# Performance work log

Hardware: AMD Instinct MI355X
Metric: run time of the kernel (lower is better)

## Reference

```python
import jax, jax.numpy as jnp
import numpy as np

N = 50000      # nodes
E = 800000     # edges (before self-loops)
F_IN = 128     # num_node_features
G = 128        # number of graphs in batch
NEG_SLOPE = 0.2  # PyG GATConv leaky_relu slope


def _add_self_loops(src, dst, n):
    loop = jnp.arange(n, dtype=src.dtype)
    return jnp.concatenate([src, loop]), jnp.concatenate([dst, loop])


def gcn_conv(x, W, b, src, dst, n):
    h = x @ W
    deg = jax.ops.segment_sum(jnp.ones_like(dst, dtype=h.dtype), dst, num_segments=n)
    dinv = jnp.where(deg > 0, jax.lax.rsqrt(deg), 0.0)
    norm = dinv[src] * dinv[dst]                      # [E+N]
    msg = h[src] * norm[:, None]                      # gather + scale
    return jax.ops.segment_sum(msg, dst, num_segments=n) + b


def gat_conv(x, W, att_src, att_dst, b, src, dst, n, heads, ch):
    # PyG GATConv (concat=True, self-loops added by caller)
    h = (x @ W).reshape(n, heads, ch)                 # [N,H,C]
    a_src = (h * att_src).sum(-1)                     # [N,H]
    a_dst = (h * att_dst).sum(-1)                     # [N,H]
    e = jax.nn.leaky_relu(a_src[src] + a_dst[dst], NEG_SLOPE)  # [E+N,H]
    # segment softmax over edges grouped by destination
    m = jax.ops.segment_max(e, dst, num_segments=n)   # [N,H]
    ex = jnp.exp(e - m[dst])
    s = jax.ops.segment_sum(ex, dst, num_segments=n)  # [N,H]
    alpha = ex / s[dst]                               # [E+N,H]
    msg = h[src] * alpha[:, :, None]                  # [E+N,H,C]
    out = jax.ops.segment_sum(msg, dst, num_segments=n)
    return out.reshape(n, heads * ch) + b


def setup_inputs() -> dict:
    key = jax.random.key(0)
    ks = jax.random.split(key, 16)
    p = lambda k, shape: jax.random.normal(k, shape, jnp.float32) * 0.05
    return {
        "x": jax.random.normal(ks[0], (N, F_IN), jnp.float32),
        "edge_index": jax.random.randint(ks[1], (2, E), 0, N, dtype=jnp.int32),
        "batch": jnp.sort(jax.random.randint(ks[2], (N,), 0, G, dtype=jnp.int32)),
        "W1": p(ks[3], (F_IN, 16)), "b1": jnp.zeros((16,), jnp.float32),
        "W2": p(ks[4], (16, 32)), "b2": jnp.zeros((32,), jnp.float32),
        "W3": p(ks[5], (32, 4 * 32)), "att_src3": p(ks[6], (4, 32)), "att_dst3": p(ks[7], (4, 32)), "b3": jnp.zeros((128,), jnp.float32),
        "W4": p(ks[8], (128, 8 * 32)), "att_src4": p(ks[9], (8, 32)), "att_dst4": p(ks[10], (8, 32)), "b4": jnp.zeros((256,), jnp.float32),
        "Wfc1": p(ks[11], (432, 128)), "bfc1": jnp.zeros((128,), jnp.float32),
        "Wfc2": p(ks[12], (128, 1)), "bfc2": jnp.zeros((1,), jnp.float32),
    }


def reference(x, edge_index, batch, W1, b1, W2, b2, W3, att_src3, att_dst3, b3,
              W4, att_src4, att_dst4, b4, Wfc1, bfc1, Wfc2, bfc2):
    src, dst = _add_self_loops(edge_index[0], edge_index[1], N)
    x1 = jax.nn.relu(gcn_conv(x, W1, b1, src, dst, N))
    x2 = jax.nn.relu(gcn_conv(x1, W2, b2, src, dst, N))
    x3 = jax.nn.relu(gat_conv(x2, W3, att_src3, att_dst3, b3, src, dst, N, 4, 32))
    x4 = jax.nn.relu(gat_conv(x3, W4, att_src4, att_dst4, b4, src, dst, N, 8, 32))
    x_jump = jnp.concatenate([x1, x2, x3, x4], axis=-1)   # [N,432]
    # global mean pool over graphs
    sums = jax.ops.segment_sum(x_jump, batch, num_segments=G)
    cnt = jax.ops.segment_sum(jnp.ones((N,), x_jump.dtype), batch, num_segments=G)
    x_pool = sums / jnp.maximum(cnt, 1.0)[:, None]         # [G,432]
    h = jax.nn.relu(x_pool @ Wfc1 + bfc1)
    return (h @ Wfc2 + bfc2).flatten()                     # [G]
```

## Files before the change

kernel.cpp:

```cpp
#include <hip/hip_runtime.h>
#include <hip/hip_bf16.h>

#define NN 50000
#define NE 800000
#define NG 128
#define EB ((NE + 255)/256)
#define MB1 ((NN + 15)/16)
#define PB 54
#define WB4 128
#define WB3 16

typedef unsigned short u16;
typedef unsigned int u32;
typedef unsigned char u8;
typedef float f32x4 __attribute__((ext_vector_type(4)));
typedef short s16x8 __attribute__((ext_vector_type(8)));

__device__ __forceinline__ float lrelu(float x){ return x > 0.f ? x : 0.2f*x; }
__device__ __forceinline__ u16 f2bf(float f){
    __hip_bfloat16 h = __float2bfloat16(f);
    return *(u16*)&h;
}
__device__ __forceinline__ void unpack8(uint4 t, float* f){
    f[0]=__uint_as_float(t.x<<16); f[1]=__uint_as_float(t.x&0xffff0000u);
    f[2]=__uint_as_float(t.y<<16); f[3]=__uint_as_float(t.y&0xffff0000u);
    f[4]=__uint_as_float(t.z<<16); f[5]=__uint_as_float(t.z&0xffff0000u);
    f[6]=__uint_as_float(t.w<<16); f[7]=__uint_as_float(t.w&0xffff0000u);
}
__device__ __forceinline__ void ub8(uint2 t, float* f){
    f[0]=(float)(t.x & 0xffu);      f[1]=(float)((t.x>>8) & 0xffu);
    f[2]=(float)((t.x>>16) & 0xffu); f[3]=(float)(t.x>>24);
    f[4]=(float)(t.y & 0xffu);      f[5]=(float)((t.y>>8) & 0xffu);
    f[6]=(float)((t.y>>16) & 0xffu); f[7]=(float)(t.y>>24);
}

__global__ void k_cm(const int* __restrict__ dstE, int* __restrict__ degi,
                     const float* __restrict__ x, const float* __restrict__ W1,
                     const float* __restrict__ W3, const float* __restrict__ W4,
                     u16* __restrict__ h1, float* __restrict__ pool,
                     u16* __restrict__ W3p, u16* __restrict__ W4p){
    if (blockIdx.x < EB){
        int e = blockIdx.x*256 + threadIdx.x;
        if (e < NE) atomicAdd(&degi[dstE[e]], 1);
        return;
    }
    if (blockIdx.x >= EB + MB1){
        int b2 = blockIdx.x - EB - MB1;
        if (b2 < PB){
            int idx = b2*1024 + threadIdx.x*4;
            if (idx < NG*432) *(float4*)(pool + idx) = make_float4(0.f,0.f,0.f,0.f);
        } else if (b2 < PB + WB4){
            int e = (b2 - PB)*256 + threadIdx.x;
            int k = e >> 8, n = e & 255;
            W4p[(k>>3)*2048 + n*8 + (k&7)] = f2bf(W4[e]);
        } else {
            int e = (b2 - PB - WB4)*256 + threadIdx.x;
            if (e < 4096){
                int k = e >> 7, n = e & 127;
                W3p[(k>>3)*1024 + n*8 + (k&7)] = f2bf(W3[e]);
            }
        }
        return;
    }
    __shared__ float wl[128*16];
    for (int i = threadIdx.x; i < 128*16; i += 256) wl[i] = W1[i];
    __syncthreads();
    int m  = threadIdx.x & 15;
    int nl = threadIdx.x >> 4;
    int node = (blockIdx.x - EB) * 16 + nl;
    if (node >= NN) return;
    const float* row = x + (size_t)node * 128;
    float acc = 0.f;
#pragma unroll 8
    for (int k = 0; k < 128; k++) acc += row[k] * wl[k*16 + m];
    h1[(size_t)node*16 + m] = f2bf(acc);
}

__global__ void k_scan_a(const int* __restrict__ deg, int* __restrict__ rowptr,
                         float* __restrict__ dinv, int* __restrict__ cursor,
                         int* __restrict__ bsum, int n){
    __shared__ int lds[256];
    int base = blockIdx.x*1024 + threadIdx.x*4;
    int v[4]; int s = 0;
#pragma unroll
    for (int k=0;k<4;k++){ v[k] = (base+k < n) ? deg[base+k] : 0; s += v[k]; }
    lds[threadIdx.x] = s;
    __syncthreads();
    for (int off=1; off<256; off<<=1){
        int t = (threadIdx.x>=off) ? lds[threadIdx.x-off] : 0;
        __syncthreads(); lds[threadIdx.x] += t; __syncthreads();
    }
    int run = lds[threadIdx.x] - s;
#pragma unroll
    for (int k=0;k<4;k++){
        if (base+k < n){
            rowptr[base+k] = run;
            dinv[base+k] = rsqrtf((float)(v[k] + 1));
            cursor[base+k] = 0;
        }
        run += v[k];
    }
    if (threadIdx.x == 255) bsum[blockIdx.x] = lds[255];
}

__global__ void k_scan_c(int* __restrict__ rowptr, const int* __restrict__ bsum,
                         int nb, int n){
    __shared__ int off_s;
    if (threadIdx.x < 64){
        int v = ((int)threadIdx.x < nb && (int)threadIdx.x < (int)blockIdx.x)
                ? bsum[threadIdx.x] : 0;
        for (int m=1; m<64; m<<=1) v += __shfl_xor(v, m, 64);
        if (threadIdx.x == 0) off_s = v;
    }
    __syncthreads();
    int o = off_s;
    int idx = blockIdx.x*1024 + threadIdx.x*4;
#pragma unroll
    for (int k=0;k<4;k++) if (idx+k < n) rowptr[idx+k] += o;
    if ((int)blockIdx.x == nb-1 && threadIdx.x == 0) rowptr[n] = o + bsum[nb-1];
}

__global__ void k_scatter(const int* __restrict__ src, const int* __restrict__ dst,
                          const int* __restrict__ rowptr, int* __restrict__ cursor,
                          int* __restrict__ csr_src, int E){
    int e = blockIdx.x*blockDim.x + threadIdx.x;
    if (e < E){
        int d = dst[e];
        int pos = rowptr[d] + atomicAdd(&cursor[d], 1);
        csr_src[pos] = src[e];
    }
}

__global__ void k_gcn_agg16_mm2(const u16* __restrict__ h1, const float* __restrict__ dinv,
                                const int* __restrict__ rowptr, const int* __restrict__ csr_src,
                                const float* __restrict__ b1, const float* __restrict__ W2,
                                const int* __restrict__ batch, float* __restrict__ pool,
                                u16* __restrict__ h2, int n){
    __shared__ float w2s[16*32];
    __shared__ float x1s[16][17];
    __shared__ int gbuf[16];
    for (int i = threadIdx.x; i < 512; i += 256) w2s[i] = W2[i];
    int lin = threadIdx.x & 15;
    int nl  = threadIdx.x >> 4;
    int i = blockIdx.x*16 + nl;
    int ll = lin & 1, slot = lin >> 1;
    float di = dinv[i];
    float acc[8] = {0.f,0.f,0.f,0.f,0.f,0.f,0.f,0.f};
    if (slot == 0){
        uint4 t = *(const uint4*)(h1 + (size_t)i*16 + ll*8);
        float f[8]; unpack8(t, f);
#pragma unroll
        for (int k=0;k<8;k++) acc[k] = di*f[k];
    }
    int e0 = rowptr[i], e1 = rowptr[i+1];
    int e = e0 + slot;
    for (; e + 8 < e1; e += 16){
        int j0 = csr_src[e], j1 = csr_src[e+8];
        float d0 = dinv[j0], d1 = dinv[j1];
        uint4 t0 = *(const uint4*)(h1 + (size_t)j0*16 + ll*8);
        uint4 t1 = *(const uint4*)(h1 + (size_t)j1*16 + ll*8);
        float f0[8], f1[8]; unpack8(t0, f0); unpack8(t1, f1);
#pragma unroll
        for (int k=0;k<8;k++) acc[k] += d0*f0[k] + d1*f1[k];
    }
    if (e < e1){
        int j = csr_src[e];
        float dj = dinv[j];
        uint4 t = *(const uint4*)(h1 + (size_t)j*16 + ll*8);
        float f[8]; unpack8(t, f);
#pragma unroll
        for (int k=0;k<8;k++) acc[k] += dj*f[k];
    }
#pragma unroll
    for (int m = 2; m < 16; m <<= 1){
#pragma unroll
        for (int k=0;k<8;k++) acc[k] += __shfl_xor(acc[k], m, 64);
    }
    if (slot == 0){
#pragma unroll
        for (int k=0;k<8;k++)
            x1s[nl][ll*8+k] = fmaxf(di*acc[k] + b1[ll*8+k], 0.f);
        if (lin == 0) gbuf[nl] = batch[i];
    }
    __syncthreads();
    {
        float a0 = 0.f, a1 = 0.f;
        int m0 = lin*2;
#pragma unroll
        for (int k=0;k<16;k++){
            float xv = x1s[nl][k];
            a0 += xv * w2s[k*32 + m0];
            a1 += xv * w2s[k*32 + m0 + 1];
        }
        u32 pk = (u32)f2bf(a0) | ((u32)f2bf(a1) << 16);
        *(u32*)(h2 + (size_t)i*32 + m0) = pk;
    }
    if (threadIdx.x < 16){
        int c = threadIdx.x;
        int curg = gbuf[0];
        float a = 0.f;
        for (int nd = 0; nd < 16; nd++){
            int g = gbuf[nd];
            if (g != curg){ atomicAdd(&pool[curg*432 + c], a); a = 0.f; curg = g; }
            a += x1s[nd][c];
        }
        atomicAdd(&pool[curg*432 + c], a);
    }
}

__global__ void k_gcn_agg32(const u16* __restrict__ h2, const float* __restrict__ dinv,
                            const int* __restrict__ rowptr, const int* __restrict__ csr_src,
                            const float* __restrict__ b2, const int* __restrict__ batch,
                            float* __restrict__ pool, u16* __restrict__ x2b, int n){
    __shared__ float x2s[16][33];
    __shared__ int gbuf[16];
    int lin = threadIdx.x & 15;
    int nl  = threadIdx.x >> 4;
    int i = blockIdx.x*16 + nl;
    int ll = lin & 3, slot = lin >> 2;
    float di = dinv[i];
    float acc[8] = {0.f,0.f,0.f,0.f,0.f,0.f,0.f,0.f};
    if (slot == 0){
        uint4 t = *(const uint4*)(h2 + (size_t)i*32 + ll*8);
        float f[8]; unpack8(t, f);
#pragma unroll
        for (int k=0;k<8;k++) acc[k] = di*f[k];
    }
    int e0 = rowptr[i], e1 = rowptr[i+1];
    int e = e0 + slot;
    for (; e + 12 < e1; e += 16){
        int j0 = csr_src[e], j1 = csr_src[e+4], j2 = csr_src[e+8], j3 = csr_src[e+12];
        float d0 = dinv[j0], d1 = dinv[j1], d2 = dinv[j2], d3 = dinv[j3];
        uint4 t0 = *(const uint4*)(h2 + (size_t)j0*32 + ll*8);
        uint4 t1 = *(const uint4*)(h2 + (size_t)j1*32 + ll*8);
        uint4 t2 = *(const uint4*)(h2 + (size_t)j2*32 + ll*8);
        uint4 t3 = *(const uint4*)(h2 + (size_t)j3*32 + ll*8);
        float f0[8], f1[8], f2[8], f3[8];
        unpack8(t0, f0); unpack8(t1, f1); unpack8(t2, f2); unpack8(t3, f3);
#pragma unroll
        for (int k=0;k<8;k++) acc[k] += d0*f0[k] + d1*f1[k] + d2*f2[k] + d3*f3[k];
    }
    for (; e < e1; e += 4){
        int j = csr_src[e];
        float dj = dinv[j];
        uint4 t = *(const uint4*)(h2 + (size_t)j*32 + ll*8);
        float f[8]; unpack8(t, f);
#pragma unroll
        for (int k=0;k<8;k++) acc[k] += dj*f[k];
    }
#pragma unroll
    for (int m = 4; m < 16; m <<= 1){
#pragma unroll
        for (int k=0;k<8;k++) acc[k] += __shfl_xor(acc[k], m, 64);
    }
    if (slot == 0){
        float o[8];
#pragma unroll
        for (int k=0;k<8;k++){
            o[k] = fmaxf(di*acc[k] + b2[ll*8+k], 0.f);
            x2s[nl][ll*8+k] = o[k];
        }
        uint4 pk;
        pk.x = (u32)f2bf(o[0]) | ((u32)f2bf(o[1])<<16);
        pk.y = (u32)f2bf(o[2]) | ((u32)f2bf(o[3])<<16);
        pk.z = (u32)f2bf(o[4]) | ((u32)f2bf(o[5])<<16);
        pk.w = (u32)f2bf(o[6]) | ((u32)f2bf(o[7])<<16);
        *(uint4*)(x2b + (size_t)i*32 + ll*8) = pk;
        if (lin == 0) gbuf[nl] = batch[i];
    }
    __syncthreads();
    if (threadIdx.x < 32){
        int c = threadIdx.x;
        int curg = gbuf[0];
        float a = 0.f;
        for (int nd = 0; nd < 16; nd++){
            int g = gbuf[nd];
            if (g != curg){ atomicAdd(&pool[curg*432 + 16 + c], a); a = 0.f; curg = g; }
            a += x2s[nd][c];
        }
        atomicAdd(&pool[curg*432 + 16 + c], a);
    }
}

__global__ void k_mm3_mfma(const u16* __restrict__ x2b, const u16* __restrict__ W3p,
                           const float* __restrict__ as, const float* __restrict__ adt,
                           u16* __restrict__ hb, float* __restrict__ asrc,
                           float* __restrict__ adst){
    __shared__ u16 outS[64][136];
    __shared__ float asS[128], adS[128];
    int tid = threadIdx.x;
    int lane = tid & 63, w = tid >> 6;
    int nbase = blockIdx.x * 64;
    if (tid < 128){ asS[tid] = as[tid]; adS[tid] = adt[tid]; }
    int q = lane >> 4, r16 = lane & 15;
    int m = nbase + w*16 + r16;
    f32x4 acc[8] = {};
    s16x8 af = (s16x8){0,0,0,0,0,0,0,0};
    if (m < NN) af = *(const s16x8*)(x2b + (size_t)m*32 + q*8);
#pragma unroll
    for (int t = 0; t < 8; t++){
        s16x8 bf = *(const s16x8*)(W3p + q*1024 + (t*16 + r16)*8);
        acc[t] = __builtin_amdgcn_mfma_f32_16x16x32_bf16(af, bf, acc[t], 0, 0, 0);
    }
#pragma unroll
    for (int t = 0; t < 8; t++){
#pragma unroll
        for (int r = 0; r < 4; r++){
            outS[w*16 + q*4 + r][t*16 + r16] = f2bf(acc[t][r]);
        }
    }
    __syncthreads();
    {
        int row = w*16 + r16;
        int node = nbase + row;
        float ps = 0.f, pd = 0.f;
        const u16* orow = &outS[row][q*32];
#pragma unroll
        for (int c = 0; c < 32; c++){
            float f = __uint_as_float(((u32)orow[c]) << 16);
            ps += f * asS[q*32 + c];
            pd += f * adS[q*32 + c];
        }
        if (node < NN){
            asrc[(size_t)node*4 + q] = ps;
            adst[(size_t)node*4 + q] = pd;
        }
    }
    for (int idx = tid; idx < 1024; idx += 256){
        int row = idx >> 4, seg = idx & 15;
        int node = nbase + row;
        if (node < NN){
            uint4 v = *(const uint4*)&outS[row][seg*8];
            *(uint4*)(hb + (size_t)node*128 + seg*8) = v;
        }
    }
}

__global__ void k_mm4_mfma(const u16* __restrict__ x3b, const u16* __restrict__ W4p,
                           const float* __restrict__ as, const float* __restrict__ adt,
                           u8* __restrict__ hb, float* __restrict__ scl,
                           float* __restrict__ asrc, float* __restrict__ adst){
    __shared__ u16 outS[64][136];
    __shared__ float asS[128], adS[128];
    int tid = threadIdx.x;
    int lane = tid & 63, w = tid >> 6;
    int cbase = blockIdx.x * 128;
    int nbase = blockIdx.y * 64;
    if (tid < 128){ asS[tid] = as[cbase + tid]; adS[tid] = adt[cbase + tid]; }
    int q = lane >> 4, r16 = lane & 15;
    int m = nbase + w*16 + r16;
    f32x4 acc[8] = {};
    for (int s = 0; s < 4; s++){
        s16x8 af = (s16x8){0,0,0,0,0,0,0,0};
        if (m < NN) af = *(const s16x8*)(x3b + (size_t)m*128 + s*32 + q*8);
        int kb = s*4 + q;
#pragma unroll
        for (int t = 0; t < 8; t++){
            s16x8 bf = *(const s16x8*)(W4p + (size_t)kb*2048 + (cbase + t*16 + r16)*8);
            acc[t] = __builtin_amdgcn_mfma_f32_16x16x32_bf16(af, bf, acc[t], 0, 0, 0);
        }
    }
#pragma unroll
    for (int t = 0; t < 8; t++){
#pragma unroll
        for (int r = 0; r < 4; r++){
            outS[w*16 + q*4 + r][t*16 + r16] = f2bf(acc[t][r]);
        }
    }
    __syncthreads();
    {
        int row = w*16 + r16;
        int node = nbase + row;
        float ps = 0.f, pd = 0.f, mx = 0.f;
        const u16* orow = &outS[row][q*32];
#pragma unroll
        for (int c = 0; c < 32; c++){
            float f = __uint_as_float(((u32)orow[c]) << 16);
            ps += f * asS[q*32 + c];
            pd += f * adS[q*32 + c];
            mx = fmaxf(mx, fabsf(f));
        }
        if (node < NN){
            int hg = (cbase >> 5) + q;
            asrc[(size_t)node*8 + hg] = ps;
            adst[(size_t)node*8 + hg] = pd;
        }
        mx = fmaxf(mx, __shfl_xor(mx, 16, 64));
        mx = fmaxf(mx, __shfl_xor(mx, 32, 64));
        float inv = mx > 0.f ? 127.f/mx : 0.f;
        if (node < NN && q == 0) scl[(size_t)node*2 + (cbase>>7)] = mx * (1.f/127.f);
        if (node < NN){
            u32 pk_[8];
#pragma unroll
            for (int g = 0; g < 8; g++){
                u32 v = 0;
#pragma unroll
                for (int kk = 0; kk < 4; kk++){
                    float f = __uint_as_float(((u32)orow[g*4+kk]) << 16);
                    int bq = (int)rintf(f*inv) + 128;
                    v |= ((u32)bq) << (8*kk);
                }
                pk_[g] = v;
            }
            *(uint4*)(hb + (size_t)node*256 + cbase + q*32)      = make_uint4(pk_[0],pk_[1],pk_[2],pk_[3]);
            *(uint4*)(hb + (size_t)node*256 + cbase + q*32 + 16) = make_uint4(pk_[4],pk_[5],pk_[6],pk_[7]);
        }
    }
}

__global__ void k_gat_agg3(const u16* __restrict__ h, const float* __restrict__ asrc,
                           const float* __restrict__ adst, const int* __restrict__ rowptr,
                           const int* __restrict__ csr_src, const float* __restrict__ b,
                           const int* __restrict__ batch, float* __restrict__ pool,
                           u16* __restrict__ x3b, int n){
    constexpr int HC = 128, CL = 16, S = 4;
    __shared__ float x3s[4][128];
    __shared__ int gbuf[4];
    int lane = threadIdx.x & 63;
    int wid  = threadIdx.x >> 6;
    int i = blockIdx.x*4 + wid;
    int ll   = lane % CL;
    int slot = lane / CL;
    int head = (ll*8)/32;
    float ad = adst[(size_t)i*4 + head];
    float acc[8] = {0.f,0.f,0.f,0.f,0.f,0.f,0.f,0.f};
    float s = 0.f;
    if (slot == 0){
        float wself = __expf(lrelu(asrc[(size_t)i*4 + head] + ad));
        uint4 t = ((const uint4*)(h + (size_t)i*HC))[ll];
        float f[8]; unpack8(t, f);
#pragma unroll
        for (int k=0;k<8;k++) acc[k] = wself*f[k];
        s = wself;
    }
    int e0 = rowptr[i], e1 = rowptr[i+1];
    int e = e0 + slot;
    for (; e + 3*S < e1; e += 4*S){
        int j0 = csr_src[e], j1 = csr_src[e+S], j2 = csr_src[e+2*S], j3 = csr_src[e+3*S];
        float w0 = __expf(lrelu(asrc[(size_t)j0*4 + head] + ad));
        float w1 = __expf(lrelu(asrc[(size_t)j1*4 + head] + ad));
        float w2 = __expf(lrelu(asrc[(size_t)j2*4 + head] + ad));
        float w3 = __expf(lrelu(asrc[(size_t)j3*4 + head] + ad));
        uint4 t0 = ((const uint4*)(h + (size_t)j0*HC))[ll];
        uint4 t1 = ((const uint4*)(h + (size_t)j1*HC))[ll];
        uint4 t2 = ((const uint4*)(h + (size_t)j2*HC))[ll];
        uint4 t3 = ((const uint4*)(h + (size_t)j3*HC))[ll];
        float f0[8], f1[8], f2[8], f3[8];
        unpack8(t0, f0); unpack8(t1, f1); unpack8(t2, f2); unpack8(t3, f3);
#pragma unroll
        for (int k=0;k<8;k++) acc[k] += w0*f0[k] + w1*f1[k] + w2*f2[k] + w3*f3[k];
        s += w0 + w1 + w2 + w3;
    }
    for (; e < e1; e += S){
        int j = csr_src[e];
        float w = __expf(lrelu(asrc[(size_t)j*4 + head] + ad));
        uint4 t = ((const uint4*)(h + (size_t)j*HC))[ll];
        float f[8]; unpack8(t, f);
#pragma unroll
        for (int k=0;k<8;k++) acc[k] += w*f[k];
        s += w;
    }
#pragma unroll
    for (int m = CL; m < 64; m <<= 1){
        s += __shfl_xor(s, m, 64);
#pragma unroll
        for (int k=0;k<8;k++) acc[k] += __shfl_xor(acc[k], m, 64);
    }
    if (slot == 0){
        float inv = 1.f / s;
        float o[8];
#pragma unroll
        for (int k=0;k<8;k++){
            o[k] = fmaxf(acc[k]*inv + b[ll*8+k], 0.f);
            x3s[wid][ll*8+k] = o[k];
        }
        uint4 pk;
        pk.x = (u32)f2bf(o[0]) | ((u32)f2bf(o[1])<<16);
        pk.y = (u32)f2bf(o[2]) | ((u32)f2bf(o[3])<<16);
        pk.z = (u32)f2bf(o[4]) | ((u32)f2bf(o[5])<<16);
        pk.w = (u32)f2bf(o[6]) | ((u32)f2bf(o[7])<<16);
        *(uint4*)(x3b + (size_t)i*128 + ll*8) = pk;
        if (ll == 0) gbuf[wid] = batch[i];
    }
    __syncthreads();
    if (threadIdx.x < 128){
        int c = threadIdx.x;
        int g0 = gbuf[0];
        float sum = 0.f;
#pragma unroll
        for (int wd = 0; wd < 4; wd++){
            float v = x3s[wd][c];
            int gw = gbuf[wd];
            if (gw == g0) sum += v;
            else atomicAdd(&pool[gw*432 + 48 + c], v);
        }
        atomicAdd(&pool[g0*432 + 48 + c], sum);
    }
}

__global__ void k_gat_agg4(const u8* __restrict__ h, const float* __restrict__ scl,
                           const float* __restrict__ asrc, const float* __restrict__ adst,
                           const int* __restrict__ rowptr, const int* __restrict__ csr_src,
                           const float* __restrict__ b, const int* __restrict__ batch,
                           float* __restrict__ pool){
    constexpr int S = 2;
    __shared__ float x4buf[4][256];
    __shared__ int gbuf[4];
    int lane = threadIdx.x & 63;
    int wid  = threadIdx.x >> 6;
    int i = blockIdx.x*4 + wid;
    int ll   = lane & 31;
    int slot = lane >> 5;
    int head = ll >> 2;
    int half = ll >> 4;
    float ad = adst[(size_t)i*8 + head];
    float acc[8] = {0.f,0.f,0.f,0.f,0.f,0.f,0.f,0.f};
    float s = 0.f, cw = 0.f;
    if (slot == 0){
        float w = __expf(lrelu(asrc[(size_t)i*8 + head] + ad));
        float ws = w * scl[(size_t)i*2 + half];
        uint2 t = *(const uint2*)(h + (size_t)i*256 + ll*8);
        float f[8]; ub8(t, f);
#pragma unroll
        for (int k=0;k<8;k++) acc[k] = ws*f[k];
        s = w; cw = ws;
    }
    int e0 = rowptr[i], e1 = rowptr[i+1];
    int e = e0 + slot;
    for (; e + 3*S < e1; e += 4*S){
        int j0 = csr_src[e], j1 = csr_src[e+S], j2 = csr_src[e+2*S], j3 = csr_src[e+3*S];
        float w0 = __expf(lrelu(asrc[(size_t)j0*8 + head] + ad));
        float w1 = __expf(lrelu(asrc[(size_t)j1*8 + head] + ad));
        float w2 = __expf(lrelu(asrc[(size_t)j2*8 + head] + ad));
        float w3 = __expf(lrelu(asrc[(size_t)j3*8 + head] + ad));
        float ws0 = w0 * scl[(size_t)j0*2 + half];
        float ws1 = w1 * scl[(size_t)j1*2 + half];
        float ws2 = w2 * scl[(size_t)j2*2 + half];
        float ws3 = w3 * scl[(size_t)j3*2 + half];
        uint2 t0 = *(const uint2*)(h + (size_t)j0*256 + ll*8);
        uint2 t1 = *(const uint2*)(h + (size_t)j1*256 + ll*8);
        uint2 t2 = *(const uint2*)(h + (size_t)j2*256 + ll*8);
        uint2 t3 = *(const uint2*)(h + (size_t)j3*256 + ll*8);
        float f0[8], f1[8], f2[8], f3[8];
        ub8(t0, f0); ub8(t1, f1); ub8(t2, f2); ub8(t3, f3);
#pragma unroll
        for (int k=0;k<8;k++) acc[k] += ws0*f0[k] + ws1*f1[k] + ws2*f2[k] + ws3*f3[k];
        s += w0 + w1 + w2 + w3;
        cw += ws0 + ws1 + ws2 + ws3;
    }
    for (; e < e1; e += S){
        int j = csr_src[e];
        float w = __expf(lrelu(asrc[(size_t)j*8 + head] + ad));
        float ws = w * scl[(size_t)j*2 + half];
        uint2 t = *(const uint2*)(h + (size_t)j*256 + ll*8);
        float f[8]; ub8(t, f);
#pragma unroll
        for (int k=0;k<8;k++) acc[k] += ws*f[k];
        s += w; cw += ws;
    }
#pragma unroll
    for (int k=0;k<8;k++) acc[k] -= 128.f*cw;
    s += __shfl_xor(s, 32, 64);
#pragma unroll
    for (int k=0;k<8;k++) acc[k] += __shfl_xor(acc[k], 32, 64);
    if (slot == 0){
        float inv = 1.f / s;
#pragma unroll
        for (int k=0;k<8;k++)
            x4buf[wid][ll*8+k] = fmaxf(acc[k]*inv + b[ll*8+k], 0.f);
        if (ll == 0) gbuf[wid] = batch[i];
    }
    __syncthreads();
    {
        int c = threadIdx.x;
        int g0 = gbuf[0];
        float sum = 0.f;
#pragma unroll
        for (int wd = 0; wd < 4; wd++){
            float v = x4buf[wd][c];
            int gw = gbuf[wd];
            if (gw == g0) sum += v;
            else atomicAdd(&pool[gw*432 + 176 + c], v);
        }
        atomicAdd(&pool[g0*432 + 176 + c], sum);
    }
}

__global__ void k_fc(const float* __restrict__ pool, const int* __restrict__ batch,
                     const float* __restrict__ Wf1, const float* __restrict__ bf1,
                     const float* __restrict__ Wf2, const float* __restrict__ bf2,
                     float* __restrict__ out){
    int g = blockIdx.x, j = threadIdx.x;
    int lo = 0, hi = NN;
    while (lo < hi){ int mid = (lo+hi) >> 1; if (batch[mid] < g) lo = mid+1; else hi = mid; }
    int s0 = lo;
    lo = 0; hi = NN;
    while (lo < hi){ int mid = (lo+hi) >> 1; if (batch[mid] < g+1) lo = mid+1; else hi = mid; }
    int cnt = lo - s0;
    float invc = 1.f / (float)max(cnt, 1);
    float acc = 0.f;
    for (int k = 0; k < 432; k++) acc += pool[g*432 + k] * Wf1[k*128 + j];
    float hv = fmaxf(acc * invc + bf1[j], 0.f);
    float p = hv * Wf2[j];
    for (int off = 32; off > 0; off >>= 1) p += __shfl_down(p, off, 64);
    __shared__ float part[2];
    if ((j & 63) == 0) part[j >> 6] = p;
    __syncthreads();
    if (j == 0) out[g] = part[0] + part[1] + bf2[0];
}

extern "C" void kernel_launch(void* const* d_in, const int* in_sizes, int n_in,
                              void* d_out, int out_size, void* d_ws, size_t ws_size,
                              hipStream_t stream){
    const float* x     = (const float*)d_in[0];
    const int*   ei    = (const int*)  d_in[1];
    const int*   batch = (const int*)  d_in[2];
    const float* W1 = (const float*)d_in[3];  const float* b1 = (const float*)d_in[4];
    const float* W2 = (const float*)d_in[5];  const float* b2 = (const float*)d_in[6];
    const float* W3 = (const float*)d_in[7];
    const float* as3 = (const float*)d_in[8]; const float* ad3 = (const float*)d_in[9];
    const float* b3 = (const float*)d_in[10];
    const float* W4 = (const float*)d_in[11];
    const float* as4 = (const float*)d_in[12]; const float* ad4 = (const float*)d_in[13];
    const float* b4 = (const float*)d_in[14];
    const float* Wf1 = (const float*)d_in[15]; const float* bf1 = (const float*)d_in[16];
    const float* Wf2 = (const float*)d_in[17]; const float* bf2 = (const float*)d_in[18];
    float* out = (float*)d_out;

    const int* srcE = ei;
    const int* dstE = ei + NE;

    char* base = (char*)d_ws; size_t off = 0;
    auto alloc = [&](size_t bytes)->void*{
        void* p = base + off;
        off += (bytes + 255) & ~(size_t)255;
        return p;
    };
    int*   degi    = (int*)  alloc((size_t)NN*4);
    int*   cursor  = (int*)  alloc((size_t)NN*4);
    float* dinv    = (float*)alloc((size_t)NN*4);
    int*   rowptr  = (int*)  alloc((size_t)(NN+1)*4);
    int*   bsum    = (int*)  alloc(64*4);
    int*   csr_src = (int*)  alloc((size_t)NE*4);
    u16*   h1b     = (u16*)  alloc((size_t)NN*16*2);
    u16*   h2b     = (u16*)  alloc((size_t)NN*32*2);
    u16*   hb3     = (u16*)  alloc((size_t)NN*128*2);
    u8*    hb4     = (u8*)   alloc((size_t)NN*256);
    float* scl4    = (float*)alloc((size_t)NN*2*4);
    u16*   x2b     = (u16*)  alloc((size_t)NN*32*2);
    u16*   x3b     = (u16*)  alloc((size_t)NN*128*2);
    u16*   W3p     = (u16*)  alloc((size_t)4096*2);
    u16*   W4p     = (u16*)  alloc((size_t)32768*2);
    float* a_src   = (float*)alloc((size_t)NN*8*4);
    float* a_dst   = (float*)alloc((size_t)NN*8*4);
    float* pool    = (float*)alloc((size_t)NG*432*4);

    hipMemsetAsync(degi, 0, (size_t)NN*4, stream);

    const int SB = (NN + 1023)/1024;

    k_cm     <<<EB + MB1 + PB + WB4 + WB3, 256, 0, stream>>>(dstE, degi, x, W1, W3, W4,
                                                             h1b, pool, W3p, W4p);
    k_scan_a <<<SB, 256, 0, stream>>>(degi, rowptr, dinv, cursor, bsum, NN);
    k_scan_c <<<SB, 256, 0, stream>>>(rowptr, bsum, SB, NN);
    k_scatter<<<EB, 256, 0, stream>>>(srcE, dstE, rowptr, cursor, csr_src, NE);

    k_gcn_agg16_mm2<<<NN/16, 256, 0, stream>>>(h1b, dinv, rowptr, csr_src, b1, W2,
                                               batch, pool, h2b, NN);

    k_gcn_agg32<<<NN/16, 256, 0, stream>>>(h2b, dinv, rowptr, csr_src, b2, batch,
                                           pool, x2b, NN);

    k_mm3_mfma<<<(NN+63)/64, 256, 0, stream>>>(x2b, W3p, as3, ad3, hb3, a_src, a_dst);
    k_gat_agg3<<<NN/4, 256, 0, stream>>>(hb3, a_src, a_dst, rowptr, csr_src, b3,
                                         batch, pool, x3b, NN);

    {
        dim3 grid(2, (NN + 63)/64);
        k_mm4_mfma<<<grid, 256, 0, stream>>>(x3b, W4p, as4, ad4, hb4, scl4, a_src, a_dst);
    }
    k_gat_agg4<<<NN/4, 256, 0, stream>>>(hb4, scl4, a_src, a_dst, rowptr, csr_src, b4,
                                         batch, pool);

    k_fc<<<NG, 128, 0, stream>>>(pool, batch, Wf1, bf1, Wf2, bf2, out);
}
```

Baseline: 375.4 us.

## Quantize GAT layer-3 features to int8 with per-node scale; vectorize first matmul

The layer-3 GAT features are stored as int8 with a per-node scale, replacing bf16. This halves the bytes gathered per edge during attention aggregation, with the +128 offset removed through a weighted-scale correction term. Separately, the first dense matmul now uses a transposed LDS weight layout and float4 loads of x. The node bounds check is dropped there, which relies on the grid covering exactly NN nodes. Int8 quantization adds rounding error to the layer-3 messages.

```diff
diff --git a/kernel.cpp b/kernel.cpp
--- a/kernel.cpp
+++ b/kernel.cpp
@@ -62,17 +62,23 @@
         }
         return;
     }
-    __shared__ float wl[128*16];
-    for (int i = threadIdx.x; i < 128*16; i += 256) wl[i] = W1[i];
+    __shared__ float wlT[16][132];
+    for (int i = threadIdx.x; i < 2048; i += 256){
+        int k = i >> 4, m = i & 15;
+        wlT[m][k] = W1[i];
+    }
     __syncthreads();
     int m  = threadIdx.x & 15;
     int nl = threadIdx.x >> 4;
     int node = (blockIdx.x - EB) * 16 + nl;
-    if (node >= NN) return;
-    const float* row = x + (size_t)node * 128;
+    const float4* row4 = (const float4*)(x + (size_t)node * 128);
     float acc = 0.f;
-#pragma unroll 8
-    for (int k = 0; k < 128; k++) acc += row[k] * wl[k*16 + m];
+#pragma unroll
+    for (int k4 = 0; k4 < 32; k4++){
+        float4 xv = row4[k4];
+        const float* wv = &wlT[m][k4*4];
+        acc += xv.x*wv[0] + xv.y*wv[1] + xv.z*wv[2] + xv.w*wv[3];
+    }
     h1[(size_t)node*16 + m] = f2bf(acc);
 }
 
@@ -284,8 +290,8 @@
 
 __global__ void k_mm3_mfma(const u16* __restrict__ x2b, const u16* __restrict__ W3p,
                            const float* __restrict__ as, const float* __restrict__ adt,
-                           u16* __restrict__ hb, float* __restrict__ asrc,
-                           float* __restrict__ adst){
+                           u8* __restrict__ hb, float* __restrict__ scl,
+                           float* __restrict__ asrc, float* __restrict__ adst){
     __shared__ u16 outS[64][136];
     __shared__ float asS[128], adS[128];
     int tid = threadIdx.x;
@@ -313,25 +319,38 @@
     {
         int row = w*16 + r16;
         int node = nbase + row;
-        float ps = 0.f, pd = 0.f;
+        float ps = 0.f, pd = 0.f, mx = 0.f;
         const u16* orow = &outS[row][q*32];
 #pragma unroll
         for (int c = 0; c < 32; c++){
             float f = __uint_as_float(((u32)orow[c]) << 16);
             ps += f * asS[q*32 + c];
             pd += f * adS[q*32 + c];
+            mx = fmaxf(mx, fabsf(f));
         }
         if (node < NN){
             asrc[(size_t)node*4 + q] = ps;
             adst[(size_t)node*4 + q] = pd;
         }
-    }
-    for (int idx = tid; idx < 1024; idx += 256){
-        int row = idx >> 4, seg = idx & 15;
-        int node = nbase + row;
+        mx = fmaxf(mx, __shfl_xor(mx, 16, 64));
+        mx = fmaxf(mx, __shfl_xor(mx, 32, 64));
+        float inv = mx > 0.f ? 127.f/mx : 0.f;
+        if (node < NN && q == 0) scl[node] = mx * (1.f/127.f);
         if (node < NN){
-            uint4 v = *(const uint4*)&outS[row][seg*8];
-            *(uint4*)(hb + (size_t)node*128 + seg*8) = v;
+            u32 pk_[8];
+#pragma unroll
+            for (int g = 0; g < 8; g++){
+                u32 v = 0;
+#pragma unroll
+                for (int kk = 0; kk < 4; kk++){
+                    float f = __uint_as_float(((u32)orow[g*4+kk]) << 16);
+                    int bq = (int)rintf(f*inv) + 128;
+                    v |= ((u32)bq) << (8*kk);
+                }
+                pk_[g] = v;
+            }
+            *(uint4*)(hb + (size_t)node*128 + q*32)      = make_uint4(pk_[0],pk_[1],pk_[2],pk_[3]);
+            *(uint4*)(hb + (size_t)node*128 + q*32 + 16) = make_uint4(pk_[4],pk_[5],pk_[6],pk_[7]);
         }
     }
 }
@@ -408,12 +427,12 @@
     }
 }
 
-__global__ void k_gat_agg3(const u16* __restrict__ h, const float* __restrict__ asrc,
-                           const float* __restrict__ adst, const int* __restrict__ rowptr,
-                           const int* __restrict__ csr_src, const float* __restrict__ b,
-                           const int* __restrict__ batch, float* __restrict__ pool,
-                           u16* __restrict__ x3b, int n){
-    constexpr int HC = 128, CL = 16, S = 4;
+__global__ void k_gat_agg3(const u8* __restrict__ h, const float* __restrict__ scl,
+                           const float* __restrict__ asrc, const float* __restrict__ adst,
+                           const int* __restrict__ rowptr, const int* __restrict__ csr_src,
+                           const float* __restrict__ b, const int* __restrict__ batch,
+                           float* __restrict__ pool, u16* __restrict__ x3b, int n){
+    constexpr int CL = 16, S = 4;
     __shared__ float x3s[4][128];
     __shared__ int gbuf[4];
     int lane = threadIdx.x & 63;
@@ -424,14 +443,15 @@
     int head = (ll*8)/32;
     float ad = adst[(size_t)i*4 + head];
     float acc[8] = {0.f,0.f,0.f,0.f,0.f,0.f,0.f,0.f};
-    float s = 0.f;
+    float s = 0.f, cw = 0.f;
     if (slot == 0){
-        float wself = __expf(lrelu(asrc[(size_t)i*4 + head] + ad));
-        uint4 t = ((const uint4*)(h + (size_t)i*HC))[ll];
-        float f[8]; unpack8(t, f);
-#pragma unroll
-        for (int k=0;k<8;k++) acc[k] = wself*f[k];
-        s = wself;
+        float w = __expf(lrelu(asrc[(size_t)i*4 + head] + ad));
+        float ws = w * scl[i];
+        uint2 t = *(const uint2*)(h + (size_t)i*128 + ll*8);
+        float f[8]; ub8(t, f);
+#pragma unroll
+        for (int k=0;k<8;k++) acc[k] = ws*f[k];
+        s = w; cw = ws;
     }
     int e0 = rowptr[i], e1 = rowptr[i+1];
     int e = e0 + slot;
@@ -441,25 +461,33 @@
         float w1 = __expf(lrelu(asrc[(size_t)j1*4 + head] + ad));
         float w2 = __expf(lrelu(asrc[(size_t)j2*4 + head] + ad));
         float w3 = __expf(lrelu(asrc[(size_t)j3*4 + head] + ad));
-        uint4 t0 = ((const uint4*)(h + (size_t)j0*HC))[ll];
-        uint4 t1 = ((const uint4*)(h + (size_t)j1*HC))[ll];
-        uint4 t2 = ((const uint4*)(h + (size_t)j2*HC))[ll];
-        uint4 t3 = ((const uint4*)(h + (size_t)j3*HC))[ll];
+        float ws0 = w0 * scl[j0];
+        float ws1 = w1 * scl[j1];
+        float ws2 = w2 * scl[j2];
+        float ws3 = w3 * scl[j3];
+        uint2 t0 = *(const uint2*)(h + (size_t)j0*128 + ll*8);
+        uint2 t1 = *(const uint2*)(h + (size_t)j1*128 + ll*8);
+        uint2 t2 = *(const uint2*)(h + (size_t)j2*128 + ll*8);
+        uint2 t3 = *(const uint2*)(h + (size_t)j3*128 + ll*8);
         float f0[8], f1[8], f2[8], f3[8];
-        unpack8(t0, f0); unpack8(t1, f1); unpack8(t2, f2); unpack8(t3, f3);
-#pragma unroll
-        for (int k=0;k<8;k++) acc[k] += w0*f0[k] + w1*f1[k] + w2*f2[k] + w3*f3[k];
+        ub8(t0, f0); ub8(t1, f1); ub8(t2, f2); ub8(t3, f3);
+#pragma unroll
+        for (int k=0;k<8;k++) acc[k] += ws0*f0[k] + ws1*f1[k] + ws2*f2[k] + ws3*f3[k];
         s += w0 + w1 + w2 + w3;
+        cw += ws0 + ws1 + ws2 + ws3;
     }
     for (; e < e1; e += S){
         int j = csr_src[e];
         float w = __expf(lrelu(asrc[(size_t)j*4 + head] + ad));
-        uint4 t = ((const uint4*)(h + (size_t)j*HC))[ll];
-        float f[8]; unpack8(t, f);
-#pragma unroll
-        for (int k=0;k<8;k++) acc[k] += w*f[k];
-        s += w;
-    }
+        float ws = w * scl[j];
+        uint2 t = *(const uint2*)(h + (size_t)j*128 + ll*8);
+        float f[8]; ub8(t, f);
+#pragma unroll
+        for (int k=0;k<8;k++) acc[k] += ws*f[k];
+        s += w; cw += ws;
+    }
+#pragma unroll
+    for (int k=0;k<8;k++) acc[k] -= 128.f*cw;
 #pragma unroll
     for (int m = CL; m < 64; m <<= 1){
         s += __shfl_xor(s, m, 64);
@@ -644,7 +672,8 @@
     int*   csr_src = (int*)  alloc((size_t)NE*4);
     u16*   h1b     = (u16*)  alloc((size_t)NN*16*2);
     u16*   h2b     = (u16*)  alloc((size_t)NN*32*2);
-    u16*   hb3     = (u16*)  alloc((size_t)NN*128*2);
+    u8*    hb3     = (u8*)   alloc((size_t)NN*128);
+    float* scl3    = (float*)alloc((size_t)NN*4);
     u8*    hb4     = (u8*)   alloc((size_t)NN*256);
     float* scl4    = (float*)alloc((size_t)NN*2*4);
     u16*   x2b     = (u16*)  alloc((size_t)NN*32*2);
@@ -671,8 +700,8 @@
     k_gcn_agg32<<<NN/16, 256, 0, stream>>>(h2b, dinv, rowptr, csr_src, b2, batch,
                                            pool, x2b, NN);
 
-    k_mm3_mfma<<<(NN+63)/64, 256, 0, stream>>>(x2b, W3p, as3, ad3, hb3, a_src, a_dst);
-    k_gat_agg3<<<NN/4, 256, 0, stream>>>(hb3, a_src, a_dst, rowptr, csr_src, b3,
+    k_mm3_mfma<<<(NN+63)/64, 256, 0, stream>>>(x2b, W3p, as3, ad3, hb3, scl3, a_src, a_dst);
+    k_gat_agg3<<<NN/4, 256, 0, stream>>>(hb3, scl3, a_src, a_dst, rowptr, csr_src, b3,
                                          batch, pool, x3b, NN);
 
     {
```

New measurement: 371.8 us. Within noise of the previous version (-1.0%).

## Aggregate layer-3 GAT on 32-wide inputs and apply W3 after aggregation

Applied to the files above, without the earlier changes.

Removes the separate layer-3 projection kernel. Attention logits are computed by folding W3 into the attention vectors (W3·att), done in k_gcn_agg32's epilogue. The GAT aggregation now gathers 32-wide bf16 x2 rows instead of 128-wide projected rows, and applies the per-head W3 slice to the aggregated result in LDS. The intent is less gather traffic and one fewer launch and intermediate buffer, paid for with a 16KB W3 LDS load per block and extra FMA work per node. Separately, the layer-1 matmul in k_cm now stages x and a transposed W1 in LDS and reads them as float4.

```diff
diff --git a/kernel.cpp b/kernel.cpp
--- a/kernel.cpp
+++ b/kernel.cpp
@@ -8,7 +8,6 @@
 #define MB1 ((NN + 15)/16)
 #define PB 54
 #define WB4 128
-#define WB3 16
 
 typedef unsigned short u16;
 typedef unsigned int u32;
@@ -37,8 +36,9 @@
 __global__ void k_cm(const int* __restrict__ dstE, int* __restrict__ degi,
                      const float* __restrict__ x, const float* __restrict__ W1,
                      const float* __restrict__ W3, const float* __restrict__ W4,
+                     const float* __restrict__ as3, const float* __restrict__ ad3,
                      u16* __restrict__ h1, float* __restrict__ pool,
-                     u16* __restrict__ W3p, u16* __restrict__ W4p){
+                     u16* __restrict__ W4p, float* __restrict__ asd3){
     if (blockIdx.x < EB){
         int e = blockIdx.x*256 + threadIdx.x;
         if (e < NE) atomicAdd(&degi[dstE[e]], 1);
@@ -54,26 +54,40 @@
             int k = e >> 8, n = e & 255;
             W4p[(k>>3)*2048 + n*8 + (k&7)] = f2bf(W4[e]);
         } else {
-            int e = (b2 - PB - WB4)*256 + threadIdx.x;
-            if (e < 4096){
-                int k = e >> 7, n = e & 127;
-                W3p[(k>>3)*1024 + n*8 + (k&7)] = f2bf(W3[e]);
-            }
+            int t = threadIdx.x;
+            int t2 = t & 127;
+            int h = t2 >> 5, k = t2 & 31;
+            const float* av = (t < 128) ? as3 : ad3;
+            float v = 0.f;
+#pragma unroll
+            for (int c = 0; c < 32; c++)
+                v += W3[k*128 + h*32 + c] * av[h*32 + c];
+            asd3[t] = v;
         }
         return;
     }
-    __shared__ float wl[128*16];
-    for (int i = threadIdx.x; i < 128*16; i += 256) wl[i] = W1[i];
+    __shared__ float wlT[16][132];
+    __shared__ float xs[16][132];
+    int node0 = (blockIdx.x - EB) * 16;
+    for (int i = threadIdx.x; i < 2048; i += 256){
+        int k = i >> 4, m = i & 15;
+        wlT[m][k] = W1[i];
+    }
+    for (int i = threadIdx.x; i < 512; i += 256){
+        int r = i >> 5, c = i & 31;
+        *(float4*)&xs[r][c*4] = ((const float4*)(x + (size_t)(node0 + r)*128))[c];
+    }
     __syncthreads();
     int m  = threadIdx.x & 15;
     int nl = threadIdx.x >> 4;
-    int node = (blockIdx.x - EB) * 16 + nl;
-    if (node >= NN) return;
-    const float* row = x + (size_t)node * 128;
     float acc = 0.f;
-#pragma unroll 8
-    for (int k = 0; k < 128; k++) acc += row[k] * wl[k*16 + m];
-    h1[(size_t)node*16 + m] = f2bf(acc);
+#pragma unroll
+    for (int k4 = 0; k4 < 32; k4++){
+        float4 xv = *(const float4*)&xs[nl][k4*4];
+        float4 wv = *(const float4*)&wlT[m][k4*4];
+        acc += xv.x*wv.x + xv.y*wv.y + xv.z*wv.z + xv.w*wv.w;
+    }
+    h1[(size_t)(node0 + nl)*16 + m] = f2bf(acc);
 }
 
 __global__ void k_scan_a(const int* __restrict__ deg, int* __restrict__ rowptr,
@@ -211,9 +225,13 @@
 __global__ void k_gcn_agg32(const u16* __restrict__ h2, const float* __restrict__ dinv,
                             const int* __restrict__ rowptr, const int* __restrict__ csr_src,
                             const float* __restrict__ b2, const int* __restrict__ batch,
-                            float* __restrict__ pool, u16* __restrict__ x2b, int n){
+                            const float* __restrict__ asd3, float* __restrict__ pool,
+                            u16* __restrict__ x2b, float* __restrict__ asrc3,
+                            float* __restrict__ adst3, int n){
     __shared__ float x2s[16][33];
+    __shared__ float asdS[256];
     __shared__ int gbuf[16];
+    asdS[threadIdx.x] = asd3[threadIdx.x];
     int lin = threadIdx.x & 15;
     int nl  = threadIdx.x >> 4;
     int i = blockIdx.x*16 + nl;
@@ -279,60 +297,122 @@
             a += x2s[nd][c];
         }
         atomicAdd(&pool[curg*432 + 16 + c], a);
-    }
-}
-
-__global__ void k_mm3_mfma(const u16* __restrict__ x2b, const u16* __restrict__ W3p,
-                           const float* __restrict__ as, const float* __restrict__ adt,
-                           u16* __restrict__ hb, float* __restrict__ asrc,
-                           float* __restrict__ adst){
-    __shared__ u16 outS[64][136];
-    __shared__ float asS[128], adS[128];
+    } else if (threadIdx.x < 160){
+        int t = threadIdx.x - 32;
+        int nd = t >> 3, r = t & 7;
+        int h = r & 3;
+        const float* A = &asdS[(r >= 4 ? 128 : 0) + h*32];
+        float v = 0.f;
+#pragma unroll
+        for (int k = 0; k < 32; k++) v += x2s[nd][k] * A[k];
+        int node = blockIdx.x*16 + nd;
+        if (r >= 4) adst3[(size_t)node*4 + h] = v;
+        else        asrc3[(size_t)node*4 + h] = v;
+    }
+}
+
+__global__ void k_gat_agg3(const u16* __restrict__ x2b, const float* __restrict__ asrc,
+                           const float* __restrict__ adst, const int* __restrict__ rowptr,
+                           const int* __restrict__ csr_src, const float* __restrict__ W3,
+                           const float* __restrict__ b, const int* __restrict__ batch,
+                           float* __restrict__ pool, u16* __restrict__ x3b, int n){
+    __shared__ float W3s[32][128];
+    __shared__ float aggS[4][4][32];
+    __shared__ float x3s[4][128];
+    __shared__ int gbuf[4];
     int tid = threadIdx.x;
-    int lane = tid & 63, w = tid >> 6;
-    int nbase = blockIdx.x * 64;
-    if (tid < 128){ asS[tid] = as[tid]; adS[tid] = adt[tid]; }
-    int q = lane >> 4, r16 = lane & 15;
-    int m = nbase + w*16 + r16;
-    f32x4 acc[8] = {};
-    s16x8 af = (s16x8){0,0,0,0,0,0,0,0};
-    if (m < NN) af = *(const s16x8*)(x2b + (size_t)m*32 + q*8);
-#pragma unroll
-    for (int t = 0; t < 8; t++){
-        s16x8 bf = *(const s16x8*)(W3p + q*1024 + (t*16 + r16)*8);
-        acc[t] = __builtin_amdgcn_mfma_f32_16x16x32_bf16(af, bf, acc[t], 0, 0, 0);
-    }
-#pragma unroll
-    for (int t = 0; t < 8; t++){
-#pragma unroll
-        for (int r = 0; r < 4; r++){
-            outS[w*16 + q*4 + r][t*16 + r16] = f2bf(acc[t][r]);
-        }
+    for (int idx = tid; idx < 4096; idx += 256)
+        W3s[idx >> 7][idx & 127] = W3[idx];
+    int lane = tid & 63;
+    int wid  = tid >> 6;
+    int i = blockIdx.x*4 + wid;
+    int ll   = lane & 15;
+    int slot = lane >> 4;
+    int head = ll >> 2;
+    int kseg = (ll & 3) * 8;
+    float ad = adst[(size_t)i*4 + head];
+    float acc[8] = {0.f,0.f,0.f,0.f,0.f,0.f,0.f,0.f};
+    float s = 0.f;
+    if (slot == 0){
+        float w = __expf(lrelu(asrc[(size_t)i*4 + head] + ad));
+        uint4 t = *(const uint4*)(x2b + (size_t)i*32 + kseg);
+        float f[8]; unpack8(t, f);
+#pragma unroll
+        for (int k=0;k<8;k++) acc[k] = w*f[k];
+        s = w;
+    }
+    int e0 = rowptr[i], e1 = rowptr[i+1];
+    int e = e0 + slot;
+    for (; e + 12 < e1; e += 16){
+        int j0 = csr_src[e], j1 = csr_src[e+4], j2 = csr_src[e+8], j3 = csr_src[e+12];
+        float w0 = __expf(lrelu(asrc[(size_t)j0*4 + head] + ad));
+        float w1 = __expf(lrelu(asrc[(size_t)j1*4 + head] + ad));
+        float w2 = __expf(lrelu(asrc[(size_t)j2*4 + head] + ad));
+        float w3 = __expf(lrelu(asrc[(size_t)j3*4 + head] + ad));
+        uint4 t0 = *(const uint4*)(x2b + (size_t)j0*32 + kseg);
+        uint4 t1 = *(const uint4*)(x2b + (size_t)j1*32 + kseg);
+        uint4 t2 = *(const uint4*)(x2b + (size_t)j2*32 + kseg);
+        uint4 t3 = *(const uint4*)(x2b + (size_t)j3*32 + kseg);
+        float f0[8], f1[8], f2[8], f3[8];
+        unpack8(t0, f0); unpack8(t1, f1); unpack8(t2, f2); unpack8(t3, f3);
+#pragma unroll
+        for (int k=0;k<8;k++) acc[k] += w0*f0[k] + w1*f1[k] + w2*f2[k] + w3*f3[k];
+        s += w0 + w1 + w2 + w3;
+    }
+    for (; e < e1; e += 4){
+        int j = csr_src[e];
+        float w = __expf(lrelu(asrc[(size_t)j*4 + head] + ad));
+        uint4 t = *(const uint4*)(x2b + (size_t)j*32 + kseg);
+        float f[8]; unpack8(t, f);
+#pragma unroll
+        for (int k=0;k<8;k++) acc[k] += w*f[k];
+        s += w;
+    }
+#pragma unroll
+    for (int m = 16; m < 64; m <<= 1){
+        s += __shfl_xor(s, m, 64);
+#pragma unroll
+        for (int k=0;k<8;k++) acc[k] += __shfl_xor(acc[k], m, 64);
+    }
+    if (slot == 0){
+        float inv = 1.f / s;
+        float o[8];
+#pragma unroll
+        for (int k=0;k<8;k++) o[k] = acc[k]*inv;
+        *(float4*)&aggS[wid][head][kseg]     = make_float4(o[0],o[1],o[2],o[3]);
+        *(float4*)&aggS[wid][head][kseg + 4] = make_float4(o[4],o[5],o[6],o[7]);
+        if (ll == 0) gbuf[wid] = batch[i];
     }
     __syncthreads();
     {
-        int row = w*16 + r16;
-        int node = nbase + row;
-        float ps = 0.f, pd = 0.f;
-        const u16* orow = &outS[row][q*32];
-#pragma unroll
-        for (int c = 0; c < 32; c++){
-            float f = __uint_as_float(((u32)orow[c]) << 16);
-            ps += f * asS[q*32 + c];
-            pd += f * adS[q*32 + c];
-        }
-        if (node < NN){
-            asrc[(size_t)node*4 + q] = ps;
-            adst[(size_t)node*4 + q] = pd;
-        }
-    }
-    for (int idx = tid; idx < 1024; idx += 256){
-        int row = idx >> 4, seg = idx & 15;
-        int node = nbase + row;
-        if (node < NN){
-            uint4 v = *(const uint4*)&outS[row][seg*8];
-            *(uint4*)(hb + (size_t)node*128 + seg*8) = v;
-        }
+        int c0 = lane*2;
+        const float* ag = aggS[wid][lane >> 4];
+        float a0 = 0.f, a1 = 0.f;
+#pragma unroll
+        for (int k = 0; k < 32; k++){
+            float av = ag[k];
+            a0 += av * W3s[k][c0];
+            a1 += av * W3s[k][c0+1];
+        }
+        float o0 = fmaxf(a0 + b[c0],   0.f);
+        float o1 = fmaxf(a1 + b[c0+1], 0.f);
+        x3s[wid][c0] = o0; x3s[wid][c0+1] = o1;
+        u32 pk = (u32)f2bf(o0) | ((u32)f2bf(o1) << 16);
+        *(u32*)(x3b + (size_t)i*128 + c0) = pk;
+    }
+    __syncthreads();
+    if (tid < 128){
+        int c = tid;
+        int g0 = gbuf[0];
+        float sum = 0.f;
+#pragma unroll
+        for (int wd = 0; wd < 4; wd++){
+            float v = x3s[wd][c];
+            int gw = gbuf[wd];
+            if (gw == g0) sum += v;
+            else atomicAdd(&pool[gw*432 + 48 + c], v);
+        }
+        atomicAdd(&pool[g0*432 + 48 + c], sum);
     }
 }
 
@@ -405,96 +485,6 @@
             *(uint4*)(hb + (size_t)node*256 + cbase + q*32)      = make_uint4(pk_[0],pk_[1],pk_[2],pk_[3]);
             *(uint4*)(hb + (size_t)node*256 + cbase + q*32 + 16) = make_uint4(pk_[4],pk_[5],pk_[6],pk_[7]);
         }
-    }
-}
-
-__global__ void k_gat_agg3(const u16* __restrict__ h, const float* __restrict__ asrc,
-                           const float* __restrict__ adst, const int* __restrict__ rowptr,
-                           const int* __restrict__ csr_src, const float* __restrict__ b,
-                           const int* __restrict__ batch, float* __restrict__ pool,
-                           u16* __restrict__ x3b, int n){
-    constexpr int HC = 128, CL = 16, S = 4;
-    __shared__ float x3s[4][128];
-    __shared__ int gbuf[4];
-    int lane = threadIdx.x & 63;
-    int wid  = threadIdx.x >> 6;
-    int i = blockIdx.x*4 + wid;
-    int ll   = lane % CL;
-    int slot = lane / CL;
-    int head = (ll*8)/32;
-    float ad = adst[(size_t)i*4 + head];
-    float acc[8] = {0.f,0.f,0.f,0.f,0.f,0.f,0.f,0.f};
-    float s = 0.f;
-    if (slot == 0){
-        float wself = __expf(lrelu(asrc[(size_t)i*4 + head] + ad));
-        uint4 t = ((const uint4*)(h + (size_t)i*HC))[ll];
-        float f[8]; unpack8(t, f);
-#pragma unroll
-        for (int k=0;k<8;k++) acc[k] = wself*f[k];
-        s = wself;
-    }
-    int e0 = rowptr[i], e1 = rowptr[i+1];
-    int e = e0 + slot;
-    for (; e + 3*S < e1; e += 4*S){
-        int j0 = csr_src[e], j1 = csr_src[e+S], j2 = csr_src[e+2*S], j3 = csr_src[e+3*S];
-        float w0 = __expf(lrelu(asrc[(size_t)j0*4 + head] + ad));
-        float w1 = __expf(lrelu(asrc[(size_t)j1*4 + head] + ad));
-        float w2 = __expf(lrelu(asrc[(size_t)j2*4 + head] + ad));
-        float w3 = __expf(lrelu(asrc[(size_t)j3*4 + head] + ad));
-        uint4 t0 = ((const uint4*)(h + (size_t)j0*HC))[ll];
-        uint4 t1 = ((const uint4*)(h + (size_t)j1*HC))[ll];
-        uint4 t2 = ((const uint4*)(h + (size_t)j2*HC))[ll];
-        uint4 t3 = ((const uint4*)(h + (size_t)j3*HC))[ll];
-        float f0[8], f1[8], f2[8], f3[8];
-        unpack8(t0, f0); unpack8(t1, f1); unpack8(t2, f2); unpack8(t3, f3);
-#pragma unroll
-        for (int k=0;k<8;k++) acc[k] += w0*f0[k] + w1*f1[k] + w2*f2[k] + w3*f3[k];
-        s += w0 + w1 + w2 + w3;
-    }
-    for (; e < e1; e += S){
-        int j = csr_src[e];
-        float w = __expf(lrelu(asrc[(size_t)j*4 + head] + ad));
-        uint4 t = ((const uint4*)(h + (size_t)j*HC))[ll];
-        float f[8]; unpack8(t, f);
-#pragma unroll
-        for (int k=0;k<8;k++) acc[k] += w*f[k];
-        s += w;
-    }
-#pragma unroll
-    for (int m = CL; m < 64; m <<= 1){
-        s += __shfl_xor(s, m, 64);
-#pragma unroll
-        for (int k=0;k<8;k++) acc[k] += __shfl_xor(acc[k], m, 64);
-    }
-    if (slot == 0){
-        float inv = 1.f / s;
-        float o[8];
-#pragma unroll
-        for (int k=0;k<8;k++){
-            o[k] = fmaxf(acc[k]*inv + b[ll*8+k], 0.f);
-            x3s[wid][ll*8+k] = o[k];
-        }
-        uint4 pk;
-        pk.x = (u32)f2bf(o[0]) | ((u32)f2bf(o[1])<<16);
-        pk.y = (u32)f2bf(o[2]) | ((u32)f2bf(o[3])<<16);
-        pk.z = (u32)f2bf(o[4]) | ((u32)f2bf(o[5])<<16);
-        pk.w = (u32)f2bf(o[6]) | ((u32)f2bf(o[7])<<16);
-        *(uint4*)(x3b + (size_t)i*128 + ll*8) = pk;
-        if (ll == 0) gbuf[wid] = batch[i];
-    }
-    __syncthreads();
-    if (threadIdx.x < 128){
-        int c = threadIdx.x;
-        int g0 = gbuf[0];
-        float sum = 0.f;
-#pragma unroll
-        for (int wd = 0; wd < 4; wd++){
-            float v = x3s[wd][c];
-            int gw = gbuf[wd];
-            if (gw == g0) sum += v;
-            else atomicAdd(&pool[gw*432 + 48 + c], v);
-        }
-        atomicAdd(&pool[g0*432 + 48 + c], sum);
     }
 }
 
@@ -644,13 +634,12 @@
     int*   csr_src = (int*)  alloc((size_t)NE*4);
     u16*   h1b     = (u16*)  alloc((size_t)NN*16*2);
     u16*   h2b     = (u16*)  alloc((size_t)NN*32*2);
-    u16*   hb3     = (u16*)  alloc((size_t)NN*128*2);
     u8*    hb4     = (u8*)   alloc((size_t)NN*256);
     float* scl4    = (float*)alloc((size_t)NN*2*4);
     u16*   x2b     = (u16*)  alloc((size_t)NN*32*2);
     u16*   x3b     = (u16*)  alloc((size_t)NN*128*2);
-    u16*   W3p     = (u16*)  alloc((size_t)4096*2);
     u16*   W4p     = (u16*)  alloc((size_t)32768*2);
+    float* asd3    = (float*)alloc(256*4);
     float* a_src   = (float*)alloc((size_t)NN*8*4);
     float* a_dst   = (float*)alloc((size_t)NN*8*4);
     float* pool    = (float*)alloc((size_t)NG*432*4);
@@ -659,8 +648,8 @@
 
     const int SB = (NN + 1023)/1024;
 
-    k_cm     <<<EB + MB1 + PB + WB4 + WB3, 256, 0, stream>>>(dstE, degi, x, W1, W3, W4,
-                                                             h1b, pool, W3p, W4p);
+    k_cm     <<<EB + MB1 + PB + WB4 + 1, 256, 0, stream>>>(dstE, degi, x, W1, W3, W4,
+                                                           as3, ad3, h1b, pool, W4p, asd3);
     k_scan_a <<<SB, 256, 0, stream>>>(degi, rowptr, dinv, cursor, bsum, NN);
     k_scan_c <<<SB, 256, 0, stream>>>(rowptr, bsum, SB, NN);
     k_scatter<<<EB, 256, 0, stream>>>(srcE, dstE, rowptr, cursor, csr_src, NE);
@@ -669,10 +658,9 @@
                                                batch, pool, h2b, NN);
 
     k_gcn_agg32<<<NN/16, 256, 0, stream>>>(h2b, dinv, rowptr, csr_src, b2, batch,
-                                           pool, x2b, NN);
-
-    k_mm3_mfma<<<(NN+63)/64, 256, 0, stream>>>(x2b, W3p, as3, ad3, hb3, a_src, a_dst);
-    k_gat_agg3<<<NN/4, 256, 0, stream>>>(hb3, a_src, a_dst, rowptr, csr_src, b3,
+                                           asd3, pool, x2b, a_src, a_dst, NN);
+
+    k_gat_agg3<<<NN/4, 256, 0, stream>>>(x2b, a_src, a_dst, rowptr, csr_src, W3, b3,
                                          batch, pool, x3b, NN);
 
     {
```

Result: no change. 375.0 us (-0.1%).
